# Kernel tuning notes

Measured on AMD Instinct MI355X. Metric: run time of the kernel, lower is better.

The kernel has to match this reference:

```python
import jax, jax.numpy as jnp
import numpy as np

B = 16384
F = 256  # num_features
H1, H2 = 64, 32  # hidden_units


def setup_inputs() -> dict:
    key = jax.random.key(0)
    kx, k1, kb1, k2, kb2, k3, kb3 = jax.random.split(key, 7)
    x = jax.random.normal(kx, (B, F), dtype=jnp.float32)
    # Stacked per-feature MLP params (torch Linear-style fan-in init scale).
    W1 = jax.random.normal(k1, (F, 1, H1), dtype=jnp.float32) * 1.0      # fan_in=1
    b1 = jax.random.normal(kb1, (F, H1), dtype=jnp.float32) * 0.1
    W2 = jax.random.normal(k2, (F, H1, H2), dtype=jnp.float32) * (1.0 / np.sqrt(H1))
    b2 = jax.random.normal(kb2, (F, H2), dtype=jnp.float32) * 0.1
    W3 = jax.random.normal(k3, (F, H2, 1), dtype=jnp.float32) * (1.0 / np.sqrt(H2))
    b3 = jax.random.normal(kb3, (F, 1), dtype=jnp.float32) * 0.1
    bias = jnp.zeros((1,), dtype=jnp.float32)
    return {"x": x, "W1": W1, "b1": b1, "W2": W2, "b2": b2,
            "W3": W3, "b3": b3, "bias": bias}


def reference(x, W1, b1, W2, b2, W3, b3, bias):
    # All F independent 1->64->32->1 MLPs batched as grouped GEMMs.
    # Layer 1: input dim is 1, so it's an outer-product broadcast.
    h1 = jax.nn.relu(x[:, :, None] * W1[:, 0, :] + b1)          # [B, F, H1]
    h2 = jax.nn.relu(jnp.einsum('bfh,fhk->bfk', h1, W2) + b2)   # [B, F, H2]
    contributions = jnp.einsum('bfk,fko->bfo', h2, W3)[..., 0] + b3[:, 0]  # [B, F]
    logits = bias[0] + contributions.sum(axis=1)                # [B]
    probs = jax.nn.sigmoid(logits)
    return logits, probs
```

## Files before the change

### kernel.cpp

```cpp
#include <hip/hip_runtime.h>
#include <math.h>


#define NAM_B 16384
#define NAM_F 256
#define FPW   16
#define NFS   (NAM_F / FPW)
#define RPW   64
#define WPB   8
#define NBLK  ((NAM_B / RPW) * NFS / WPB)

typedef __attribute__((ext_vector_type(8))) _Float16 f16x8;
typedef __attribute__((ext_vector_type(4))) _Float16 f16x4;
typedef __attribute__((ext_vector_type(2))) _Float16 f16x2;
typedef __attribute__((ext_vector_type(4))) float    f32x4;

union pk8 { f16x8 v; f16x2 h[4]; };
union h2u { f16x2 h; unsigned u; };

__global__ __launch_bounds__(256) void nam_prep(
    const float* __restrict__ x,  const float* __restrict__ W2,
    const float* __restrict__ W1, const float* __restrict__ b1,
    _Float16* __restrict__ xT, _Float16* __restrict__ w2p,
    _Float16* __restrict__ w1p, _Float16* __restrict__ b1p) {
    __shared__ float xs[64][65];
    const int b = blockIdx.x;
    const int t = threadIdx.x;
    if (b < 1024) {
        const int r0 = (b & 255) * 64;
        const int c0 = (b >> 8) * 64;
        const int rr = t >> 4;
        const int cc = (t & 15) * 4;
        #pragma unroll
        for (int e = 0; e < 4; ++e) {
            const float4 v = *reinterpret_cast<const float4*>(
                x + (size_t)(r0 + rr + e*16) * NAM_F + c0 + cc);
            xs[rr + e*16][cc+0] = v.x; xs[rr + e*16][cc+1] = v.y;
            xs[rr + e*16][cc+2] = v.z; xs[rr + e*16][cc+3] = v.w;
        }
        __syncthreads();
        const int wc = t >> 4;
        const int j  = (t & 15) * 4;
        #pragma unroll
        for (int e = 0; e < 4; ++e) {
            const int c = wc + e*16;
            f16x4 o = {(_Float16)xs[j+0][c], (_Float16)xs[j+1][c],
                       (_Float16)xs[j+2][c], (_Float16)xs[j+3][c]};
            *reinterpret_cast<f16x4*>(xT + (size_t)(c0 + c) * NAM_B + r0 + j) = o;
        }
    } else {
        const int f = b - 1024;
        const int s = t >> 7, a = (t >> 6) & 1, L = t & 63;
        const int hi = L >> 4, m = L & 15;
        const float* __restrict__ W2f = W2 + (size_t)f * (64*32);
        f16x8 o;
        #pragma unroll
        for (int j = 0; j < 8; ++j)
            o[j] = (_Float16)W2f[(s*32 + hi*8 + j)*32 + a*16 + m];
        *reinterpret_cast<f16x8*>(w2p + ((size_t)(f*4 + s*2 + a)*64 + L) * 8) = o;
        if (t < 16) {
            const int which = t >> 3;
            const int s2 = (t >> 2) & 1, hi2 = t & 3;
            const float* __restrict__ src =
                (which ? b1 : W1) + f*64 + s2*32 + hi2*8;
            f16x8 o2;
            #pragma unroll
            for (int j = 0; j < 8; ++j) o2[j] = (_Float16)src[j];
            _Float16* dst = (which ? b1p : w1p) + ((size_t)(f*2 + s2)*4 + hi2)*8;
            *reinterpret_cast<f16x8*>(dst) = o2;
        }
    }
}

__global__ __launch_bounds__(512, 4) void nam_main(
    const float* __restrict__ b2, const float* __restrict__ W3,
    const float* __restrict__ b3,
    const _Float16* __restrict__ xT, const _Float16* __restrict__ w2p,
    const _Float16* __restrict__ w1p, const _Float16* __restrict__ b1p,
    float* __restrict__ partial) {
    const int t = threadIdx.x;
    const int w = t >> 6, lane = t & 63;
    const int hi = lane >> 4, m = lane & 15;
    const int fs  = blockIdx.x >> 5;
    const int r0  = ((blockIdx.x & 31) * WPB + w) * RPW;
    const int fbase = fs * FPW;

    const f16x8* __restrict__ wp8 = reinterpret_cast<const f16x8*>(w2p);
    const f16x2 hzero = {(_Float16)0.f, (_Float16)0.f};
    const unsigned short* __restrict__ xu =
        reinterpret_cast<const unsigned short*>(xT);

    float rs[4] = {0.f, 0.f, 0.f, 0.f};
    float b3sum = 0.f;

    unsigned xv = xu[(size_t)fbase * NAM_B + r0 + lane];

    #pragma unroll 2
    for (int i = 0; i < FPW; ++i) {
        const int f = fbase + i;
        const int inext = (i + 1 < FPW) ? (i + 1) : (FPW - 1);
        const unsigned xv_n = xu[(size_t)(fbase + inext) * NAM_B + r0 + lane];

        const f16x8 a00 = wp8[(size_t)(f*4 + 0)*64 + lane];
        const f16x8 a01 = wp8[(size_t)(f*4 + 1)*64 + lane];
        const f16x8 a10 = wp8[(size_t)(f*4 + 2)*64 + lane];
        const f16x8 a11 = wp8[(size_t)(f*4 + 3)*64 + lane];
        pk8 w10, w11, b10, b11;
        w10.v = *reinterpret_cast<const f16x8*>(w1p + ((size_t)(f*2+0)*4 + hi)*8);
        w11.v = *reinterpret_cast<const f16x8*>(w1p + ((size_t)(f*2+1)*4 + hi)*8);
        b10.v = *reinterpret_cast<const f16x8*>(b1p + ((size_t)(f*2+0)*4 + hi)*8);
        b11.v = *reinterpret_cast<const f16x8*>(b1p + ((size_t)(f*2+1)*4 + hi)*8);
        const f32x4 b2v0 = *reinterpret_cast<const f32x4*>(b2 + f*32 + hi*4);
        const f32x4 b2v1 = *reinterpret_cast<const f32x4*>(b2 + f*32 + 16 + hi*4);
        const f32x4 w3v0 = *reinterpret_cast<const f32x4*>(W3 + f*32 + hi*4);
        const f32x4 w3v1 = *reinterpret_cast<const f32x4*>(W3 + f*32 + 16 + hi*4);
        b3sum += b3[f];

        #pragma unroll
        for (int sub = 0; sub < 4; ++sub) {
            h2u xb;
            const unsigned bits = (unsigned)__shfl((int)xv, sub*16 + m);
            xb.u = bits * 0x10001u;
            pk8 bf0, bf1;
            #pragma unroll
            for (int u = 0; u < 4; ++u) {
                bf0.h[u] = __builtin_elementwise_max(xb.h * w10.h[u] + b10.h[u], hzero);
                bf1.h[u] = __builtin_elementwise_max(xb.h * w11.h[u] + b11.h[u], hzero);
            }
            f32x4 acc0 = __builtin_amdgcn_mfma_f32_16x16x32_f16(a00, bf0.v, b2v0, 0,0,0);
            acc0       = __builtin_amdgcn_mfma_f32_16x16x32_f16(a10, bf1.v, acc0, 0,0,0);
            f32x4 acc1 = __builtin_amdgcn_mfma_f32_16x16x32_f16(a01, bf0.v, b2v1, 0,0,0);
            acc1       = __builtin_amdgcn_mfma_f32_16x16x32_f16(a11, bf1.v, acc1, 0,0,0);
            float ts = 0.f;
            #pragma unroll
            for (int r = 0; r < 4; ++r) {
                ts = fmaf(fmaxf(acc0[r], 0.f), w3v0[r], ts);
                ts = fmaf(fmaxf(acc1[r], 0.f), w3v1[r], ts);
            }
            ts += __shfl_xor(ts, 16);
            ts += __shfl_xor(ts, 32);
            rs[sub] += ts;
        }
        xv = xv_n;
    }

    float vsel = (lane < 16) ? rs[0] : (lane < 32) ? rs[1]
               : (lane < 48) ? rs[2] : rs[3];
    partial[(size_t)fs * NAM_B + r0 + lane] = vsel + b3sum;
}

__global__ __launch_bounds__(256) void nam_merge(
    const float* __restrict__ partial, const float* __restrict__ bias,
    float* __restrict__ out) {
    const int r = blockIdx.x * 256 + threadIdx.x;
    float s = bias[0];
    #pragma unroll
    for (int g = 0; g < NFS; ++g) s += partial[(size_t)g * NAM_B + r];
    out[r] = s;
    out[NAM_B + r] = 1.0f / (1.0f + expf(-s));
}

extern "C" void kernel_launch(void* const* d_in, const int* in_sizes, int n_in,
                              void* d_out, int out_size, void* d_ws, size_t ws_size,
                              hipStream_t stream) {
    const float* x    = (const float*)d_in[0];
    const float* W1   = (const float*)d_in[1];
    const float* b1   = (const float*)d_in[2];
    const float* W2   = (const float*)d_in[3];
    const float* b2   = (const float*)d_in[4];
    const float* W3   = (const float*)d_in[5];
    const float* b3   = (const float*)d_in[6];
    const float* bias = (const float*)d_in[7];
    float* out = (float*)d_out;

    _Float16* xT  = (_Float16*)d_ws;
    _Float16* w2p = xT  + (size_t)NAM_F * NAM_B;
    _Float16* w1p = w2p + (size_t)NAM_F * 64 * 32;
    _Float16* b1p = w1p + (size_t)NAM_F * 64;
    float* partial = (float*)(b1p + (size_t)NAM_F * 64);

    nam_prep<<<dim3(1280), 256, 0, stream>>>(x, W2, W1, b1, xT, w2p, w1p, b1p);
    nam_main<<<dim3(NBLK), 512, 0, stream>>>(b2, W3, b3, xT, w2p, w1p, b1p, partial);
    nam_merge<<<dim3(NAM_B / 256), 256, 0, stream>>>(partial, bias, out);
}
```

Measured before the change: 114.1 us.

## Drop x transpose pass; read x rows directly in main kernel with fewer features per wave

Removes the prep-stage transpose of x into a half-precision feature-major buffer. The main kernel now loads each lane's 8 contiguous float features with two float4 reads and broadcasts them with shuffles. Features per wave drop from 16 to 8, which doubles the number of blocks and the partial-sum rows, and the occupancy hint rises to 6. The aim is to cut the transpose kernel's memory traffic and its write/read round trip, at the cost of strided row loads from x and a larger merge.

```diff
diff --git a/kernel.cpp b/kernel.cpp
--- a/kernel.cpp
+++ b/kernel.cpp
@@ -4,103 +4,71 @@
 
 #define NAM_B 16384
 #define NAM_F 256
-#define FPW   16
+#define FPW   8
 #define NFS   (NAM_F / FPW)
 #define RPW   64
 #define WPB   8
 #define NBLK  ((NAM_B / RPW) * NFS / WPB)
 
 typedef __attribute__((ext_vector_type(8))) _Float16 f16x8;
-typedef __attribute__((ext_vector_type(4))) _Float16 f16x4;
 typedef __attribute__((ext_vector_type(2))) _Float16 f16x2;
 typedef __attribute__((ext_vector_type(4))) float    f32x4;
 
 union pk8 { f16x8 v; f16x2 h[4]; };
-union h2u { f16x2 h; unsigned u; };
 
 __global__ __launch_bounds__(256) void nam_prep(
-    const float* __restrict__ x,  const float* __restrict__ W2,
-    const float* __restrict__ W1, const float* __restrict__ b1,
-    _Float16* __restrict__ xT, _Float16* __restrict__ w2p,
-    _Float16* __restrict__ w1p, _Float16* __restrict__ b1p) {
-    __shared__ float xs[64][65];
-    const int b = blockIdx.x;
+    const float* __restrict__ W2, const float* __restrict__ W1,
+    const float* __restrict__ b1,
+    _Float16* __restrict__ w2p, _Float16* __restrict__ w1p,
+    _Float16* __restrict__ b1p) {
+    const int f = blockIdx.x;
     const int t = threadIdx.x;
-    if (b < 1024) {
-        const int r0 = (b & 255) * 64;
-        const int c0 = (b >> 8) * 64;
-        const int rr = t >> 4;
-        const int cc = (t & 15) * 4;
+    const int s = t >> 7, a = (t >> 6) & 1, L = t & 63;
+    const int hi = L >> 4, m = L & 15;
+    const float* __restrict__ W2f = W2 + (size_t)f * (64*32);
+    f16x8 o;
+    #pragma unroll
+    for (int j = 0; j < 8; ++j)
+        o[j] = (_Float16)W2f[(s*32 + hi*8 + j)*32 + a*16 + m];
+    *reinterpret_cast<f16x8*>(w2p + ((size_t)(f*4 + s*2 + a)*64 + L) * 8) = o;
+    if (t < 16) {
+        const int which = t >> 3;
+        const int s2 = (t >> 2) & 1, hi2 = t & 3;
+        const float* __restrict__ src = (which ? b1 : W1) + f*64 + s2*32 + hi2*8;
+        f16x8 o2;
         #pragma unroll
-        for (int e = 0; e < 4; ++e) {
-            const float4 v = *reinterpret_cast<const float4*>(
-                x + (size_t)(r0 + rr + e*16) * NAM_F + c0 + cc);
-            xs[rr + e*16][cc+0] = v.x; xs[rr + e*16][cc+1] = v.y;
-            xs[rr + e*16][cc+2] = v.z; xs[rr + e*16][cc+3] = v.w;
-        }
-        __syncthreads();
-        const int wc = t >> 4;
-        const int j  = (t & 15) * 4;
-        #pragma unroll
-        for (int e = 0; e < 4; ++e) {
-            const int c = wc + e*16;
-            f16x4 o = {(_Float16)xs[j+0][c], (_Float16)xs[j+1][c],
-                       (_Float16)xs[j+2][c], (_Float16)xs[j+3][c]};
-            *reinterpret_cast<f16x4*>(xT + (size_t)(c0 + c) * NAM_B + r0 + j) = o;
-        }
-    } else {
-        const int f = b - 1024;
-        const int s = t >> 7, a = (t >> 6) & 1, L = t & 63;
-        const int hi = L >> 4, m = L & 15;
-        const float* __restrict__ W2f = W2 + (size_t)f * (64*32);
-        f16x8 o;
-        #pragma unroll
-        for (int j = 0; j < 8; ++j)
-            o[j] = (_Float16)W2f[(s*32 + hi*8 + j)*32 + a*16 + m];
-        *reinterpret_cast<f16x8*>(w2p + ((size_t)(f*4 + s*2 + a)*64 + L) * 8) = o;
-        if (t < 16) {
-            const int which = t >> 3;
-            const int s2 = (t >> 2) & 1, hi2 = t & 3;
-            const float* __restrict__ src =
-                (which ? b1 : W1) + f*64 + s2*32 + hi2*8;
-            f16x8 o2;
-            #pragma unroll
-            for (int j = 0; j < 8; ++j) o2[j] = (_Float16)src[j];
-            _Float16* dst = (which ? b1p : w1p) + ((size_t)(f*2 + s2)*4 + hi2)*8;
-            *reinterpret_cast<f16x8*>(dst) = o2;
-        }
+        for (int j = 0; j < 8; ++j) o2[j] = (_Float16)src[j];
+        _Float16* dst = (which ? b1p : w1p) + ((size_t)(f*2 + s2)*4 + hi2)*8;
+        *reinterpret_cast<f16x8*>(dst) = o2;
     }
 }
 
-__global__ __launch_bounds__(512, 4) void nam_main(
-    const float* __restrict__ b2, const float* __restrict__ W3,
-    const float* __restrict__ b3,
-    const _Float16* __restrict__ xT, const _Float16* __restrict__ w2p,
-    const _Float16* __restrict__ w1p, const _Float16* __restrict__ b1p,
+__global__ __launch_bounds__(512, 6) void nam_main(
+    const float* __restrict__ x,  const float* __restrict__ b2,
+    const float* __restrict__ W3, const float* __restrict__ b3,
+    const _Float16* __restrict__ w2p, const _Float16* __restrict__ w1p,
+    const _Float16* __restrict__ b1p,
     float* __restrict__ partial) {
     const int t = threadIdx.x;
     const int w = t >> 6, lane = t & 63;
     const int hi = lane >> 4, m = lane & 15;
-    const int fs  = blockIdx.x >> 5;
-    const int r0  = ((blockIdx.x & 31) * WPB + w) * RPW;
+    const int fs = blockIdx.x >> 5;
+    const int r0 = ((blockIdx.x & 31) * WPB + w) * RPW;
     const int fbase = fs * FPW;
 
     const f16x8* __restrict__ wp8 = reinterpret_cast<const f16x8*>(w2p);
     const f16x2 hzero = {(_Float16)0.f, (_Float16)0.f};
-    const unsigned short* __restrict__ xu =
-        reinterpret_cast<const unsigned short*>(xT);
+
+    const float* __restrict__ xrow = x + (size_t)(r0 + lane) * NAM_F + fbase;
+    const float4 xq0 = *reinterpret_cast<const float4*>(xrow);
+    const float4 xq1 = *reinterpret_cast<const float4*>(xrow + 4);
 
     float rs[4] = {0.f, 0.f, 0.f, 0.f};
     float b3sum = 0.f;
 
-    unsigned xv = xu[(size_t)fbase * NAM_B + r0 + lane];
-
-    #pragma unroll 2
+    #pragma unroll
     for (int i = 0; i < FPW; ++i) {
         const int f = fbase + i;
-        const int inext = (i + 1 < FPW) ? (i + 1) : (FPW - 1);
-        const unsigned xv_n = xu[(size_t)(fbase + inext) * NAM_B + r0 + lane];
-
         const f16x8 a00 = wp8[(size_t)(f*4 + 0)*64 + lane];
         const f16x8 a01 = wp8[(size_t)(f*4 + 1)*64 + lane];
         const f16x8 a10 = wp8[(size_t)(f*4 + 2)*64 + lane];
@@ -115,17 +83,21 @@
         const f32x4 w3v0 = *reinterpret_cast<const f32x4*>(W3 + f*32 + hi*4);
         const f32x4 w3v1 = *reinterpret_cast<const f32x4*>(W3 + f*32 + 16 + hi*4);
         b3sum += b3[f];
+        const float xf_mine = (i < 4) ? ((i & 3) == 0 ? xq0.x : (i & 3) == 1 ? xq0.y
+                                       : (i & 3) == 2 ? xq0.z : xq0.w)
+                                      : ((i & 3) == 0 ? xq1.x : (i & 3) == 1 ? xq1.y
+                                       : (i & 3) == 2 ? xq1.z : xq1.w);
 
         #pragma unroll
         for (int sub = 0; sub < 4; ++sub) {
-            h2u xb;
-            const unsigned bits = (unsigned)__shfl((int)xv, sub*16 + m);
-            xb.u = bits * 0x10001u;
+            const float xf = __shfl(xf_mine, sub*16 + m);
+            const _Float16 xh = (_Float16)xf;
+            const f16x2 xb = {xh, xh};
             pk8 bf0, bf1;
             #pragma unroll
             for (int u = 0; u < 4; ++u) {
-                bf0.h[u] = __builtin_elementwise_max(xb.h * w10.h[u] + b10.h[u], hzero);
-                bf1.h[u] = __builtin_elementwise_max(xb.h * w11.h[u] + b11.h[u], hzero);
+                bf0.h[u] = __builtin_elementwise_max(xb * w10.h[u] + b10.h[u], hzero);
+                bf1.h[u] = __builtin_elementwise_max(xb * w11.h[u] + b11.h[u], hzero);
             }
             f32x4 acc0 = __builtin_amdgcn_mfma_f32_16x16x32_f16(a00, bf0.v, b2v0, 0,0,0);
             acc0       = __builtin_amdgcn_mfma_f32_16x16x32_f16(a10, bf1.v, acc0, 0,0,0);
@@ -141,7 +113,6 @@
             ts += __shfl_xor(ts, 32);
             rs[sub] += ts;
         }
-        xv = xv_n;
     }
 
     float vsel = (lane < 16) ? rs[0] : (lane < 32) ? rs[1]
@@ -173,13 +144,12 @@
     const float* bias = (const float*)d_in[7];
     float* out = (float*)d_out;
 
-    _Float16* xT  = (_Float16*)d_ws;
-    _Float16* w2p = xT  + (size_t)NAM_F * NAM_B;
+    _Float16* w2p = (_Float16*)d_ws;
     _Float16* w1p = w2p + (size_t)NAM_F * 64 * 32;
     _Float16* b1p = w1p + (size_t)NAM_F * 64;
     float* partial = (float*)(b1p + (size_t)NAM_F * 64);
 
-    nam_prep<<<dim3(1280), 256, 0, stream>>>(x, W2, W1, b1, xT, w2p, w1p, b1p);
-    nam_main<<<dim3(NBLK), 512, 0, stream>>>(b2, W3, b3, xT, w2p, w1p, b1p, partial);
+    nam_prep<<<dim3(NAM_F), 256, 0, stream>>>(W2, W1, b1, w2p, w1p, b1p);
+    nam_main<<<dim3(NBLK), 512, 0, stream>>>(x, b2, W3, b3, w2p, w1p, b1p, partial);
     nam_merge<<<dim3(NAM_B / 256), 256, 0, stream>>>(partial, bias, out);
 }
```

After: 260.2 us. 128% more time.
